# Optimization experiments

Measured on AMD Instinct MI355X. Metric: run time of the kernel, lower is better.

The kernel has to match this reference:

```python
import jax, jax.numpy as jnp
import numpy as np

D_MODEL = 1024
H = 16
D_K = D_MODEL // H
B, S = 2, 2048


def setup_inputs() -> dict:
    key = jax.random.key(0)
    ks = jax.random.split(key, 11)
    sc = 1.0 / np.sqrt(D_MODEL)
    inp = {
        "q": jax.random.normal(ks[0], (B, S, D_MODEL), jnp.float32),
        "k": jax.random.normal(ks[1], (B, S, D_MODEL), jnp.float32),
        "v": jax.random.normal(ks[2], (B, S, D_MODEL), jnp.float32),
        "mask": jnp.ones((1, 1, S, S), dtype=bool),
        # nn.Linear weights are [out, in]; y = x @ W.T + b
        "wq_w": jax.random.normal(ks[3], (D_MODEL, D_MODEL), jnp.float32) * sc,
        "wq_b": jnp.zeros((D_MODEL,), jnp.float32),
        "wk_w": jax.random.normal(ks[4], (D_MODEL, D_MODEL), jnp.float32) * sc,
        "wk_b": jnp.zeros((D_MODEL,), jnp.float32),
        "wv_w": jax.random.normal(ks[5], (D_MODEL, D_MODEL), jnp.float32) * sc,
        "wv_b": jnp.zeros((D_MODEL,), jnp.float32),
        "wo_w": jax.random.normal(ks[6], (D_MODEL, D_MODEL), jnp.float32) * sc,
        "wo_b": jnp.zeros((D_MODEL,), jnp.float32),
    }
    return inp


def _split_heads(x):
    b, s, _ = x.shape
    return x.reshape(b, s, H, D_K).transpose(0, 2, 1, 3)  # [B,H,S,Dk]


def reference(q, k, v, mask, wq_w, wq_b, wk_w, wk_b, wv_w, wv_b, wo_w, wo_b):
    # projections (nn.Linear: x @ W.T + b)
    qh = _split_heads(q @ wq_w.T + wq_b)
    kh = _split_heads(k @ wk_w.T + wk_b)
    vh = _split_heads(v @ wv_w.T + wv_b)
    # scaled dot-product attention with additive -1e9 masking
    scores = jnp.einsum("bhqd,bhkd->bhqk", qh, kh) / jnp.sqrt(jnp.float32(D_K))
    scores = jnp.where(mask, scores, jnp.float32(-1e9))
    attn = jax.nn.softmax(scores, axis=-1)  # dropout p=0.0 -> identity
    out = jnp.einsum("bhqk,bhkd->bhqd", attn, vh)
    out = out.transpose(0, 2, 1, 3).reshape(q.shape[0], q.shape[1], D_MODEL)
    return out @ wo_w.T + wo_b
```

## Files before the change

kernel.cpp:

```cpp
#include <hip/hip_runtime.h>
#include <hip/hip_bf16.h>


typedef unsigned short u16;
typedef unsigned int u32;
typedef short s16x4 __attribute__((ext_vector_type(4)));
typedef short s16x8 __attribute__((ext_vector_type(8)));
typedef float f32x4 __attribute__((ext_vector_type(4)));
typedef unsigned int u32x2 __attribute__((ext_vector_type(2)));
typedef unsigned int u32x4 __attribute__((ext_vector_type(4)));

#define NH 16
#define SCQ 0.1803368801111204f

__device__ __forceinline__ float bf2f(u16 h) {
  u32 u = ((u32)h) << 16;
  return __builtin_bit_cast(float, u);
}
__device__ __forceinline__ u16 f2bf(float f) {
  u32 u = __builtin_bit_cast(u32, f);
  u32 r = (u + 0x7fffu + ((u >> 16) & 1u)) >> 16;
  return (u16)r;
}

__device__ __forceinline__ u32 pk2(float a, float b) {
#if __has_builtin(__builtin_amdgcn_cvt_pk_bf16_f32)
  typedef __bf16 bf2_t __attribute__((ext_vector_type(2)));
  bf2_t r = __builtin_amdgcn_cvt_pk_bf16_f32(a, b);
  return __builtin_bit_cast(u32, r);
#else
  u32 ua = __builtin_bit_cast(u32, a) + 0x8000u;
  u32 ub = __builtin_bit_cast(u32, b) + 0x8000u;
  return __builtin_amdgcn_perm(ub, ua, 0x07060302);
#endif
}

__device__ __forceinline__ void stage16(const void* g, void* l) {
  __builtin_amdgcn_global_load_lds((const __attribute__((address_space(1))) void*)g,
                                   (__attribute__((address_space(3))) void*)l,
                                   16, 0, 0);
}

#define BAR() __builtin_amdgcn_s_barrier()
#define WAITV2 asm volatile("s_waitcnt vmcnt(2)" ::: "memory")
#define WAITV0 asm volatile("s_waitcnt vmcnt(0)" ::: "memory")

__global__ __launch_bounds__(256) void convert_all(
    const float* __restrict__ q, const float* __restrict__ k,
    const float* __restrict__ v, const float* __restrict__ wq,
    const float* __restrict__ wk, const float* __restrict__ wv,
    const float* __restrict__ wo, u16* qb, u16* kb, u16* vb, u16* wqb,
    u16* wkb, u16* wvb, u16* wob) {
  const int y = blockIdx.y;
  const float* s;
  u16* d;
  int i;
  if (y < 3) {
    s = y == 0 ? q : (y == 1 ? k : v);
    d = y == 0 ? qb : (y == 1 ? kb : vb);
    i = (blockIdx.x * 256 + threadIdx.x) * 4;
  } else {
    int w = blockIdx.x >> 10, j = blockIdx.x & 1023;
    s = w == 0 ? wq : (w == 1 ? wk : (w == 2 ? wv : wo));
    d = w == 0 ? wqb : (w == 1 ? wkb : (w == 2 ? wvb : wob));
    i = (j * 256 + threadIdx.x) * 4;
  }
  f32x4 val = *(const f32x4*)(s + i);
  u32x2 o = {pk2(val[0], val[1]), pk2(val[2], val[3])};
  *(u32x2*)(d + i) = o;
}

#define GEMM_CORE(A_, W_)                                                      \
  const int tid = threadIdx.x;                                                 \
  const int lane = tid & 63;                                                   \
  const int wid = tid >> 6;                                                    \
  const int l16 = lane & 15, quad = lane >> 4;                                 \
  const int wm = (wid >> 1) * 64, wn = (wid & 1) * 64;                         \
  const int m0 = blockIdx.y * 128;                                             \
  const int n0 = blockIdx.x * 128;                                             \
  const int ra = tid >> 2;                                                     \
  const int c8 = (tid & 3) ^ (ra & 3);                                         \
  const u16* Abase = A_ + (size_t)(m0 + ra) * 1024 + c8 * 8;                   \
  const u16* A2 = Abase + (size_t)64 * 1024;                                   \
  const u16* Wbase = W_ + (size_t)(n0 + ra) * 1024 + c8 * 8;                   \
  const u16* W2 = Wbase + (size_t)64 * 1024;                                   \
  u16* ldsA = As + tid * 8;                                                    \
  u16* ldsB = Bs + tid * 8;                                                    \
  f32x4 acc[4][4];                                                             \
  _Pragma("unroll") for (int i = 0; i < 4; ++i)                                \
  _Pragma("unroll") for (int j = 0; j < 4; ++j)                                \
      acc[i][j] = (f32x4){0.f, 0.f, 0.f, 0.f};                                 \
  for (int k0 = 0; k0 < 1024; k0 += 32) {                                      \
    __syncthreads();                                                           \
    stage16(Abase + k0, ldsA);                                                 \
    stage16(A2 + k0, ldsA + 2048);                                             \
    stage16(Wbase + k0, ldsB);                                                 \
    stage16(W2 + k0, ldsB + 2048);                                             \
    __syncthreads();                                                           \
    s16x8 bfr[4];                                                              \
    _Pragma("unroll") for (int j = 0; j < 4; ++j) {                            \
      int row = wn + j * 16 + l16;                                             \
      bfr[j] = *(const s16x8*)&Bs[(row * 4 + (quad ^ (row & 3))) * 8];         \
    }                                                                          \
    _Pragma("unroll") for (int i = 0; i < 4; ++i) {                            \
      int row = wm + i * 16 + l16;                                             \
      s16x8 afr = *(const s16x8*)&As[(row * 4 + (quad ^ (row & 3))) * 8];      \
      _Pragma("unroll") for (int j = 0; j < 4; ++j)                            \
        acc[i][j] =                                                            \
            __builtin_amdgcn_mfma_f32_16x16x32_bf16(afr, bfr[j], acc[i][j],    \
                                                    0, 0, 0);                  \
    }                                                                          \
  }

__global__ __launch_bounds__(256, 3) void proj_kernel(
    const u16* __restrict__ q, const u16* __restrict__ k, const u16* __restrict__ v,
    const u16* __restrict__ wq, const u16* __restrict__ wk, const u16* __restrict__ wv,
    const float* __restrict__ bq, const float* __restrict__ bk,
    const float* __restrict__ bv,
    u16* __restrict__ Qh, u16* __restrict__ Kh, u16* __restrict__ VhT) {
  const int z = blockIdx.z;
  const u16* A_in = z == 0 ? q : (z == 1 ? k : v);
  const u16* W_in = z == 0 ? wq : (z == 1 ? wk : wv);
  const float* bias = z == 0 ? bq : (z == 1 ? bk : bv);

  __shared__ __align__(16) u16 As[128 * 32];
  __shared__ __align__(16) u16 Bs[128 * 32];

  GEMM_CORE(A_in, W_in)

  float bcol[4];
#pragma unroll
  for (int j = 0; j < 4; ++j) bcol[j] = bias[n0 + wn + j * 16 + l16];

  if (z < 2) {
    const float qs = (z == 0) ? SCQ : 1.0f;
    u16* out = (z == 0) ? Qh : Kh;
#pragma unroll
    for (int i = 0; i < 4; ++i) {
      int gm0 = m0 + wm + i * 16 + quad * 4;
      int b = gm0 >> 11, s = gm0 & 2047;
#pragma unroll
      for (int j = 0; j < 4; ++j) {
        int gn = n0 + wn + j * 16 + l16;
        int h = gn >> 6, dk = gn & 63;
        size_t base = ((size_t)(b * NH + h) * 2048 + s) * 64 + dk;
#pragma unroll
        for (int r = 0; r < 4; ++r)
          out[base + (size_t)r * 64] = f2bf((acc[i][j][r] + bcol[j]) * qs);
      }
    }
  } else {
#pragma unroll
    for (int i = 0; i < 4; ++i) {
      int gm0 = m0 + wm + i * 16 + quad * 4;
      int b = gm0 >> 11, s = gm0 & 2047;
#pragma unroll
      for (int j = 0; j < 4; ++j) {
        int gn = n0 + wn + j * 16 + l16;
        int h = gn >> 6, dk = gn & 63;
        size_t base = ((size_t)(b * NH + h) * 64 + dk) * 2048 + s;
        u32x2 pv = {pk2(acc[i][j][0] + bcol[j], acc[i][j][1] + bcol[j]),
                    pk2(acc[i][j][2] + bcol[j], acc[i][j][3] + bcol[j])};
        *(u32x2*)&VhT[base] = pv;
      }
    }
  }
}

__global__ __launch_bounds__(256, 3) void out_kernel(const u16* __restrict__ ctx,
                                                     const u16* __restrict__ wo,
                                                     const float* __restrict__ bo,
                                                     float* __restrict__ out) {
  __shared__ __align__(16) u16 As[128 * 32];
  __shared__ __align__(16) u16 Bs[128 * 32];

  GEMM_CORE(ctx, wo)

  float bcol[4];
#pragma unroll
  for (int j = 0; j < 4; ++j) bcol[j] = bo[n0 + wn + j * 16 + l16];

#pragma unroll
  for (int i = 0; i < 4; ++i) {
    int gm0 = m0 + wm + i * 16 + quad * 4;
#pragma unroll
    for (int j = 0; j < 4; ++j) {
      int gn = n0 + wn + j * 16 + l16;
#pragma unroll
      for (int r = 0; r < 4; ++r)
        out[(size_t)(gm0 + r) * 1024 + gn] = acc[i][j][r] + bcol[j];
    }
  }
}

__global__ __launch_bounds__(512, 2) void flash_kernel(const u16* __restrict__ Qh,
                                                       const u16* __restrict__ Kh,
                                                       const u16* __restrict__ VhT,
                                                       u16* __restrict__ ctx) {
  __shared__ __align__(16) u16 smem[20480];

  const int tid = threadIdx.x;
  const int lane = tid & 63;
  const int wid = tid >> 6;
  const int l16 = lane & 15, quad = lane >> 4;
  const int bh = blockIdx.x;
  const int qt = blockIdx.y;

  const u16* Qg = Qh + ((size_t)bh * 2048 + qt * 256) * 64;
  const u16* Kg = Kh + (size_t)bh * 2048 * 64;
  const u16* Vg = VhT + (size_t)bh * 64 * 2048;

  const int rq = tid >> 3;
  const int c8 = (tid & 7) ^ (rq & 7);
  const int gq = ((rq & 15) >> 2) * 8 + (rq & 3) + (((rq >> 4) & 1) << 2);
  const int ksrc = (rq & 32) + gq;

#define KSLOT(T) (smem + ((T) & 1) * 4096)
#define VSLOT(T) (smem + 8192 + ((T) % 3) * 4096)
#define ISSUE_TILE(KT)                                                        \
  {                                                                           \
    stage16(Kg + (size_t)((KT) * 64 + ksrc) * 64 + c8 * 8,                    \
            KSLOT(KT) + tid * 8);                                             \
    stage16(Vg + (size_t)rq * 2048 + (KT) * 64 + c8 * 8,                      \
            VSLOT(KT) + tid * 8);                                             \
  }

  u16* Qs = smem;
  s16x8 bq[2][2];
  for (int p = 0; p < 2; ++p) {
#pragma unroll
    for (int i = 0; i < 2; ++i)
      stage16(Qg + (size_t)(p * 128 + rq + i * 64) * 64 + c8 * 8,
              Qs + tid * 8 + i * 4096);
    __syncthreads();
    if ((wid >> 2) == p) {
#pragma unroll
      for (int ct = 0; ct < 2; ++ct) {
        int row = (wid & 3) * 32 + ct * 16 + l16;
#pragma unroll
        for (int kk = 0; kk < 2; ++kk)
          bq[ct][kk] =
              *(const s16x8*)&Qs[(row * 8 + ((kk * 4 + quad) ^ (row & 7))) * 8];
      }
    }
    asm volatile("s_waitcnt lgkmcnt(0)" ::: "memory");
    __syncthreads();
  }

  const s16x8 a1 = {0x3F80, 0x3F80, 0x3F80, 0x3F80,
                    0x3F80, 0x3F80, 0x3F80, 0x3F80};

  f32x4 lf[2];
  f32x4 oacc[4][2];
  s16x8 bp[2][4];
#pragma unroll
  for (int ct = 0; ct < 2; ++ct) lf[ct] = (f32x4){0.f, 0.f, 0.f, 0.f};
#pragma unroll
  for (int d = 0; d < 4; ++d)
#pragma unroll
    for (int ct = 0; ct < 2; ++ct) oacc[d][ct] = (f32x4){0.f, 0.f, 0.f, 0.f};

  ISSUE_TILE(0);

#pragma unroll
  for (int kt = 0; kt < 32; ++kt) {
    BAR();
    if (kt < 31) {
      ISSUE_TILE(kt + 1);
      WAITV2;
    } else {
      WAITV0;
    }
    BAR();

    const u16* Ks = KSLOT(kt);
    const u16* Vp = VSLOT(kt == 0 ? 0 : kt - 1);
    const int pc = kt & 1, pp = pc ^ 1;

#pragma unroll
    for (int c = 0; c < 2; ++c) {
      f32x4 stc[2][2];
      __builtin_amdgcn_s_setprio(1);
#pragma unroll
      for (int r2 = 0; r2 < 2; ++r2) {
        int row = (c * 2 + r2) * 16 + l16;
        s16x8 ak0 = *(const s16x8*)&Ks[(row * 8 + (quad ^ (row & 7))) * 8];
        s16x8 ak1 = *(const s16x8*)&Ks[(row * 8 + ((4 + quad) ^ (row & 7))) * 8];
#pragma unroll
        for (int ct = 0; ct < 2; ++ct) {
          f32x4 t0 = __builtin_amdgcn_mfma_f32_16x16x32_bf16(
              ak0, bq[ct][0], (f32x4){0.f, 0.f, 0.f, 0.f}, 0, 0, 0);
          stc[r2][ct] = __builtin_amdgcn_mfma_f32_16x16x32_bf16(
              ak1, bq[ct][1], t0, 0, 0, 0);
        }
      }
      __builtin_amdgcn_s_setprio(0);

#pragma unroll
      for (int r2 = 0; r2 < 2; ++r2)
#pragma unroll
        for (int ct = 0; ct < 2; ++ct)
#pragma unroll
          for (int e = 0; e < 4; ++e)
            stc[r2][ct][e] = __builtin_exp2f(stc[r2][ct][e]);
#pragma unroll
      for (int ct = 0; ct < 2; ++ct) {
        u32x4 bu = {pk2(stc[0][ct][0], stc[0][ct][1]),
                    pk2(stc[0][ct][2], stc[0][ct][3]),
                    pk2(stc[1][ct][0], stc[1][ct][1]),
                    pk2(stc[1][ct][2], stc[1][ct][3])};
        bp[pc][c * 2 + ct] = __builtin_bit_cast(s16x8, bu);
      }

      if (kt > 0) {
        __builtin_amdgcn_s_setprio(1);
#pragma unroll
        for (int ct = 0; ct < 2; ++ct)
          lf[ct] = __builtin_amdgcn_mfma_f32_16x16x32_bf16(
              a1, bp[pp][c * 2 + ct], lf[ct], 0, 0, 0);
#pragma unroll
        for (int d = 0; d < 4; ++d) {
          int row = d * 16 + l16;
          s16x8 av =
              *(const s16x8*)&Vp[(row * 8 + ((c * 4 + quad) ^ (row & 7))) * 8];
#pragma unroll
          for (int ct = 0; ct < 2; ++ct)
            oacc[d][ct] = __builtin_amdgcn_mfma_f32_16x16x32_bf16(
                av, bp[pp][c * 2 + ct], oacc[d][ct], 0, 0, 0);
        }
        __builtin_amdgcn_s_setprio(0);
      }
    }
  }

  {
    const u16* Vp = VSLOT(31);
    __builtin_amdgcn_s_setprio(1);
#pragma unroll
    for (int c = 0; c < 2; ++c) {
#pragma unroll
      for (int ct = 0; ct < 2; ++ct)
        lf[ct] = __builtin_amdgcn_mfma_f32_16x16x32_bf16(a1, bp[1][c * 2 + ct],
                                                         lf[ct], 0, 0, 0);
#pragma unroll
      for (int d = 0; d < 4; ++d) {
        int row = d * 16 + l16;
        s16x8 av =
            *(const s16x8*)&Vp[(row * 8 + ((c * 4 + quad) ^ (row & 7))) * 8];
#pragma unroll
        for (int ct = 0; ct < 2; ++ct)
          oacc[d][ct] = __builtin_amdgcn_mfma_f32_16x16x32_bf16(
              av, bp[1][c * 2 + ct], oacc[d][ct], 0, 0, 0);
      }
    }
    __builtin_amdgcn_s_setprio(0);
  }

  const int bI = bh >> 4, hh = bh & 15;
#pragma unroll
  for (int ct = 0; ct < 2; ++ct) {
    int q = wid * 32 + ct * 16 + l16;
    float inv = 1.0f / lf[ct][0];
    size_t rowbase = ((size_t)bI * 2048 + qt * 256 + q) * 1024 + hh * 64;
#pragma unroll
    for (int d = 0; d < 4; ++d) {
      int dk0 = d * 16 + quad * 4;
      u32x2 pk = {pk2(oacc[d][ct][0] * inv, oacc[d][ct][1] * inv),
                  pk2(oacc[d][ct][2] * inv, oacc[d][ct][3] * inv)};
      *(u32x2*)&ctx[rowbase + dk0] = pk;
    }
  }
#undef ISSUE_TILE
#undef KSLOT
#undef VSLOT
}

extern "C" void kernel_launch(void* const* d_in, const int* in_sizes, int n_in,
                              void* d_out, int out_size, void* d_ws, size_t ws_size,
                              hipStream_t stream) {
  const float* q = (const float*)d_in[0];
  const float* k = (const float*)d_in[1];
  const float* v = (const float*)d_in[2];
  const float* wq = (const float*)d_in[4];
  const float* bq = (const float*)d_in[5];
  const float* wk = (const float*)d_in[6];
  const float* bk = (const float*)d_in[7];
  const float* wv = (const float*)d_in[8];
  const float* bv = (const float*)d_in[9];
  const float* wo = (const float*)d_in[10];
  const float* bo = (const float*)d_in[11];

  const size_t M1 = 1024 * 1024;
  u16* ws = (u16*)d_ws;
  u16* qb = ws;
  u16* kb = ws + 4 * M1;
  u16* vb = ws + 8 * M1;
  u16* wqb = ws + 12 * M1;
  u16* wkb = ws + 13 * M1;
  u16* wvb = ws + 14 * M1;
  u16* wob = ws + 15 * M1;
  u16* Qh = ws + 16 * M1;
  u16* Kh = ws + 20 * M1;
  u16* VhT = ws + 24 * M1;
  u16* ctx = kb;

  convert_all<<<dim3(4096, 4), 256, 0, stream>>>(q, k, v, wq, wk, wv, wo, qb, kb,
                                                 vb, wqb, wkb, wvb, wob);
  proj_kernel<<<dim3(8, 32, 3), 256, 0, stream>>>(qb, kb, vb, wqb, wkb, wvb,
                                                  bq, bk, bv, Qh, Kh, VhT);
  flash_kernel<<<dim3(32, 8), 512, 0, stream>>>(Qh, Kh, VhT, ctx);
  out_kernel<<<dim3(8, 32), 256, 0, stream>>>(ctx, wob, bo, (float*)d_out);
}
```

Before: 248.8 us.

## Double-buffer LDS tiles in projection and output GEMMs to prefetch next K tile

The GEMM core now uses two LDS buffers per operand and issues global_load_lds for the next K tile before computing on the current one, waiting with vmcnt(4) so the previous tile's loads are done. This lets global memory latency overlap with the MFMA work instead of stalling at each tile load. LDS use per block doubles, which may lower occupancy for the projection and output kernels; the attention kernel is left alone.

After: 248.9 us. No clear change (+0.1%).

```diff
diff --git a/kernel.cpp b/kernel.cpp
--- a/kernel.cpp
+++ b/kernel.cpp
@@ -43,6 +43,7 @@
 
 #define BAR() __builtin_amdgcn_s_barrier()
 #define WAITV2 asm volatile("s_waitcnt vmcnt(2)" ::: "memory")
+#define WAITV4 asm volatile("s_waitcnt vmcnt(4)" ::: "memory")
 #define WAITV0 asm volatile("s_waitcnt vmcnt(0)" ::: "memory")
 
 __global__ __launch_bounds__(256) void convert_all(
@@ -84,27 +85,38 @@
   const u16* A2 = Abase + (size_t)64 * 1024;                                   \
   const u16* Wbase = W_ + (size_t)(n0 + ra) * 1024 + c8 * 8;                   \
   const u16* W2 = Wbase + (size_t)64 * 1024;                                   \
-  u16* ldsA = As + tid * 8;                                                    \
-  u16* ldsB = Bs + tid * 8;                                                    \
   f32x4 acc[4][4];                                                             \
   _Pragma("unroll") for (int i = 0; i < 4; ++i)                                \
   _Pragma("unroll") for (int j = 0; j < 4; ++j)                                \
       acc[i][j] = (f32x4){0.f, 0.f, 0.f, 0.f};                                 \
-  for (int k0 = 0; k0 < 1024; k0 += 32) {                                      \
-    __syncthreads();                                                           \
-    stage16(Abase + k0, ldsA);                                                 \
-    stage16(A2 + k0, ldsA + 2048);                                             \
-    stage16(Wbase + k0, ldsB);                                                 \
-    stage16(W2 + k0, ldsB + 2048);                                             \
-    __syncthreads();                                                           \
+    \
+  stage16(Abase, As + tid * 8);                                                \
+  stage16(A2, As + 2048 + tid * 8);                                            \
+  stage16(Wbase, Bs + tid * 8);                                                \
+  stage16(W2, Bs + 2048 + tid * 8);                                            \
+  for (int kt = 0; kt < 32; ++kt) {                                            \
+    const int bs = (kt & 1) * 4096;                                            \
+    BAR();      \
+    if (kt < 31) {                                                             \
+      const int bn = ((kt + 1) & 1) * 4096;                                    \
+      const int kn = (kt + 1) * 32;                                            \
+      stage16(Abase + kn, As + bn + tid * 8);                                  \
+      stage16(A2 + kn, As + bn + 2048 + tid * 8);                              \
+      stage16(Wbase + kn, Bs + bn + tid * 8);                                  \
+      stage16(W2 + kn, Bs + bn + 2048 + tid * 8);                              \
+      WAITV4;             \
+    } else {                                                                   \
+      WAITV0;                                                                  \
+    }                                                                          \
+    BAR();                  \
     s16x8 bfr[4];                                                              \
     _Pragma("unroll") for (int j = 0; j < 4; ++j) {                            \
       int row = wn + j * 16 + l16;                                             \
-      bfr[j] = *(const s16x8*)&Bs[(row * 4 + (quad ^ (row & 3))) * 8];         \
+      bfr[j] = *(const s16x8*)&Bs[bs + (row * 4 + (quad ^ (row & 3))) * 8];    \
     }                                                                          \
     _Pragma("unroll") for (int i = 0; i < 4; ++i) {                            \
       int row = wm + i * 16 + l16;                                             \
-      s16x8 afr = *(const s16x8*)&As[(row * 4 + (quad ^ (row & 3))) * 8];      \
+      s16x8 afr = *(const s16x8*)&As[bs + (row * 4 + (quad ^ (row & 3))) * 8]; \
       _Pragma("unroll") for (int j = 0; j < 4; ++j)                            \
         acc[i][j] =                                                            \
             __builtin_amdgcn_mfma_f32_16x16x32_bf16(afr, bfr[j], acc[i][j],    \
@@ -123,8 +135,8 @@
   const u16* W_in = z == 0 ? wq : (z == 1 ? wk : wv);
   const float* bias = z == 0 ? bq : (z == 1 ? bk : bv);
 
-  __shared__ __align__(16) u16 As[128 * 32];
-  __shared__ __align__(16) u16 Bs[128 * 32];
+  __shared__ __align__(16) u16 As[2 * 128 * 32];
+  __shared__ __align__(16) u16 Bs[2 * 128 * 32];
 
   GEMM_CORE(A_in, W_in)
 
@@ -171,8 +183,8 @@
                                                      const u16* __restrict__ wo,
                                                      const float* __restrict__ bo,
                                                      float* __restrict__ out) {
-  __shared__ __align__(16) u16 As[128 * 32];
-  __shared__ __align__(16) u16 Bs[128 * 32];
+  __shared__ __align__(16) u16 As[2 * 128 * 32];
+  __shared__ __align__(16) u16 Bs[2 * 128 * 32];
 
   GEMM_CORE(ctx, wo)
 
```
